# Kernel optimization log

Hardware: AMD Instinct MI355X
Metric: run time of the kernel (lower is better)

The kernel has to match this reference:

```python
import jax, jax.numpy as jnp
import numpy as np

N_TOKENS = 8192      # codebook size K
HIDDEN = 256         # hidden_size H
N = 8192             # batch of latent vectors (vmapped dim)
COMMITMENT_COST = 0.25


def setup_inputs() -> dict:
    key = jax.random.key(0)
    k_h, k_cb, _ = jax.random.split(key, 3)
    h = jax.random.normal(k_h, (N, HIDDEN), dtype=jnp.float32)
    # codebook initialized exactly as in __init__: normal * 0.1
    codebook = jax.random.normal(k_cb, (N_TOKENS, HIDDEN), dtype=jnp.float32) * 0.1
    temperature = jnp.ones((), dtype=jnp.float32)  # unused, API compat
    return {"h": h, "temperature": temperature, "codebook": codebook}


def reference(h, temperature, codebook):
    """Batched VQ quantization: one-hot nearest-codebook weights + commitment loss.

    h: (N, H) float32, codebook: (K, H) float32. Returns (hard (N,K), loss (N,)).
    """
    del temperature  # VQ is always hard; kept for API compatibility
    K = codebook.shape[0]
    # squared distances ||h - c||^2 = ||h||^2 - 2 h.c + ||c||^2, avoids (N,K,H) tensor
    h_sq = jnp.sum(h * h, axis=-1, keepdims=True)              # (N, 1)
    c_sq = jnp.sum(codebook * codebook, axis=-1)               # (K,)
    dists = h_sq - 2.0 * jnp.einsum('nh,kh->nk', h, codebook) + c_sq[None, :]  # (N, K)
    idx = jnp.argmin(dists, axis=-1)                           # (N,)
    hard = jax.nn.one_hot(idx, K, dtype=h.dtype)               # (N, K)
    # STE wrapping from __call__ (gradient of hard is zero anyway)
    hard = jax.lax.stop_gradient(hard)
    # commitment_loss (per token), matching the module's method
    z_q = codebook[idx]                                        # (N, H) gather
    codebook_loss = jnp.mean((jax.lax.stop_gradient(h) - z_q) ** 2, axis=-1)
    commit_loss = jnp.mean((h - jax.lax.stop_gradient(z_q)) ** 2, axis=-1)
    loss = codebook_loss + COMMITMENT_COST * commit_loss       # (N,)
    return hard, loss
```

## Files before the change

### kernel.cpp

```cpp
#include <hip/hip_runtime.h>
#include <hip/hip_bf16.h>
#include <math.h>

#define N_ROWS   8192
#define K_CODES  8192
#define H_DIM    256
#define NSPLIT2  32
#define MARGIN   5e-4f

typedef short short8 __attribute__((ext_vector_type(8)));
typedef float f32x4  __attribute__((ext_vector_type(4)));

#define C2_OFF      0
#define H2_OFF      8192
#define DISTF_OFF   16384
#define IDXF_OFF    (DISTF_OFF + 8192)
#define FCNT_OFF    (IDXF_OFF + 8192)
#define FLIST_OFF   (FCNT_OFF + 16)
#define MAXSLOT     64
#define WS_ZERO_BYTES ((size_t)(FLIST_OFF + MAXSLOT) * 4)

#define PK_AHI ((size_t)0)
#define PK_ALO ((size_t)4 << 20)
#define PK_BHI ((size_t)8 << 20)
#define PK_BLO ((size_t)12 << 20)
#define PART_BEST ((size_t)16 << 20)
#define PART_SEC  (PART_BEST + (size_t)(NSPLIT2 * N_ROWS * 4))
#define PART_IDX  (PART_SEC  + (size_t)(NSPLIT2 * N_ROWS * 4))
#define FIXP_BEST (PART_IDX  + (size_t)(NSPLIT2 * N_ROWS * 4))
#define FIXP_IDX  (FIXP_BEST + (size_t)(MAXSLOT * 64 * 8))
#define SCRATCH_BYTES ((size_t)0x1310000)

__device__ __forceinline__ void async_copy16(const void* g, void* l) {
    __builtin_amdgcn_global_load_lds(
        (const __attribute__((address_space(1))) unsigned int*)g,
        (__attribute__((address_space(3))) unsigned int*)l, 16, 0, 0);
}

__device__ __forceinline__ void conv2(float a, float b, unsigned& hi, unsigned& lo) {
    float2 p0 = make_float2(a, b);
    __hip_bfloat162 hb = __float22bfloat162_rn(p0);
    unsigned h = *(unsigned*)&hb;
    hi = h;
    float ra = a - __uint_as_float(h << 16);
    float rb = b - __uint_as_float(h & 0xFFFF0000u);
    float2 p1 = make_float2(ra, rb);
    __hip_bfloat162 lb = __float22bfloat162_rn(p1);
    lo = *(unsigned*)&lb;
}

__global__ __launch_bounds__(256) void pack_kernel(const float* __restrict__ h,
                                                   const float* __restrict__ cb,
                                                   char* __restrict__ out,
                                                   float* __restrict__ ws) {
    int w    = threadIdx.x >> 6;
    int lane = threadIdx.x & 63;
    int ln15 = lane & 15;
    int kg   = lane >> 4;
    bool isB = blockIdx.x >= 1024;
    int u = ((blockIdx.x & 1023) << 2) + w;
    int p = u >> 3, c = u & 7;
    const float* src = isB ? cb : h;
    char* hiB = out + (isB ? PK_BHI : PK_AHI);
    char* loB = out + (isB ? PK_BLO : PK_ALO);
    const float* s = src + (size_t)(p * 16 + ln15) * H_DIM + c * 32 + kg * 8;
    float4 v0 = *(const float4*)s;
    float4 v1 = *(const float4*)(s + 4);
    unsigned h0, h1, h2, h3, l0, l1, l2, l3;
    conv2(v0.x, v0.y, h0, l0);
    conv2(v0.z, v0.w, h1, l1);
    conv2(v1.x, v1.y, h2, l2);
    conv2(v1.z, v1.w, h3, l3);
    size_t off = ((size_t)u * 64 + lane) * 16;
    *(uint4*)(hiB + off) = make_uint4(h0, h1, h2, h3);
    *(uint4*)(loB + off) = make_uint4(l0, l1, l2, l3);

    float sq = v0.x*v0.x + v0.y*v0.y + v0.z*v0.z + v0.w*v0.w
             + v1.x*v1.x + v1.y*v1.y + v1.z*v1.z + v1.w*v1.w;
    sq += __shfl_xor(sq, 16, 64);
    sq += __shfl_xor(sq, 32, 64);
    if (kg == 0) {
        int row = p * 16 + ln15;
        atomicAdd(&ws[(isB ? C2_OFF : H2_OFF) + row], sq);
    }
}

__global__ __launch_bounds__(512, 2) void vq_min_kernel(const char* __restrict__ pk,
                                                        const float* __restrict__ c2g,
                                                        float* __restrict__ pbest,
                                                        float* __restrict__ psec,
                                                        int* __restrict__ pidx) {
    __shared__ __align__(16) char smem[131072];
    const int tid  = threadIdx.x;
    const int w    = tid >> 6;
    const int lane = tid & 63;
    const int ln15 = lane & 15;
    const int kg   = lane >> 4;
    const int wr   = w >> 2;
    const int wc   = w & 3;
    const int wr8  = wr * 8;
    const int wc4  = wc * 4;

    const int pA0 = blockIdx.x * 16;
    const int pB0 = blockIdx.y * 16;

    f32x4 acc[8][4];
    #pragma unroll
    for (int m = 0; m < 8; ++m)
        #pragma unroll
        for (int n = 0; n < 4; ++n) acc[m][n] = (f32x4){0.f, 0.f, 0.f, 0.f};

#define STAGE(sE, bufc) do {                                                   \
    const int ss_ = (sE);                                                      \
    const int tt_ = ss_ >> 3, cc_ = ss_ & 7;                                   \
    const char* Ab_ = pk + ((tt_ == 1) ? PK_ALO : PK_AHI);                     \
    const char* Bb_ = pk + ((tt_ == 2) ? PK_BLO : PK_BHI);                     \
    char* db_ = smem + (bufc) * 32768;                                         \
    async_copy16(Ab_ + (((size_t)(pA0 + 2*w)     * 8 + cc_) * 64 + lane) * 16, \
                 db_ + (2*w)     * 1024);                                      \
    async_copy16(Ab_ + (((size_t)(pA0 + 2*w + 1) * 8 + cc_) * 64 + lane) * 16, \
                 db_ + (2*w + 1) * 1024);                                      \
    async_copy16(Bb_ + (((size_t)(pB0 + 2*w)     * 8 + cc_) * 64 + lane) * 16, \
                 db_ + 16384 + (2*w)     * 1024);                              \
    async_copy16(Bb_ + (((size_t)(pB0 + 2*w + 1) * 8 + cc_) * 64 + lane) * 16, \
                 db_ + 16384 + (2*w + 1) * 1024);                              \
} while (0)

#define COMPUTE(bufc) do {                                                     \
    const char* sb_ = smem + (bufc) * 32768;                                   \
    short8 av[8], bv[4];                                                       \
    _Pragma("unroll")                                                          \
    for (int m = 0; m < 8; ++m)                                                \
        av[m] = *(const short8*)(sb_ + (wr8 + m) * 1024 + lane * 16);          \
    _Pragma("unroll")                                                          \
    for (int n = 0; n < 4; ++n)                                                \
        bv[n] = *(const short8*)(sb_ + 16384 + (wc4 + n) * 1024 + lane * 16);  \
    __builtin_amdgcn_s_setprio(1);                                             \
    _Pragma("unroll")                                                          \
    for (int m = 0; m < 8; ++m)                                                \
        _Pragma("unroll")                                                      \
        for (int n = 0; n < 4; ++n)                                            \
            acc[m][n] = __builtin_amdgcn_mfma_f32_16x16x32_bf16(               \
                av[m], bv[n], acc[m][n], 0, 0, 0);                             \
    __builtin_amdgcn_s_setprio(0);                                             \
} while (0)

#define ITER(sE, bufc, vm) do {                                                \
    if ((sE) + 2 < 24) STAGE((sE) + 2, ((bufc) + 2) & 3);                      \
    asm volatile("s_waitcnt vmcnt(" #vm ")" ::: "memory");                     \
    __builtin_amdgcn_sched_barrier(0);                                         \
    __builtin_amdgcn_s_barrier();                                              \
    __builtin_amdgcn_sched_barrier(0);                                         \
    COMPUTE(bufc);                                                             \
    __builtin_amdgcn_sched_barrier(0);                                         \
} while (0)

    STAGE(0, 0);
    STAGE(1, 1);

    #pragma unroll 1
    for (int sb = 0; sb < 20; sb += 4) {
        ITER(sb + 0, 0, 8);
        ITER(sb + 1, 1, 8);
        ITER(sb + 2, 2, 8);
        ITER(sb + 3, 3, 8);
    }
    ITER(20, 0, 8);
    ITER(21, 1, 8);
    ITER(22, 2, 4);
    ITER(23, 3, 0);

#undef ITER
#undef COMPUTE
#undef STAGE

    const int colbase = blockIdx.y * 256 + wc * 64;
    float cv[4];
    #pragma unroll
    for (int n = 0; n < 4; ++n) cv[n] = c2g[colbase + n * 16 + ln15];

    float* mbv = (float*)smem;
    float* msv = (float*)(smem + 4096);
    int*   miv = (int*)(smem + 8192);

    #pragma unroll
    for (int m = 0; m < 8; ++m) {
        #pragma unroll
        for (int reg = 0; reg < 4; ++reg) {
            float b = 3.4e38f, s2 = 3.4e38f;
            int   bi = 0;
            #pragma unroll
            for (int n = 0; n < 4; ++n) {
                float d = cv[n] - 2.f * acc[m][n][reg];
                int   k = colbase + n * 16 + ln15;
                if (d < b)       { s2 = b; b = d; bi = k; }
                else if (d < s2) { s2 = d; }
            }
            #pragma unroll
            for (int msk = 1; msk <= 8; msk <<= 1) {
                float ob = __shfl_xor(b, msk, 64);
                float os = __shfl_xor(s2, msk, 64);
                int   oi = __shfl_xor(bi, msk, 64);
                if (ob < b)      { s2 = fminf(b, os); b = ob; bi = oi; }
                else if (ob > b) { s2 = fminf(s2, ob); }
                else             { if (oi < bi) bi = oi; s2 = b; }
            }
            if (ln15 == 0) {
                int r = wr * 128 + m * 16 + kg * 4 + reg;
                mbv[r * 4 + wc] = b;
                msv[r * 4 + wc] = s2;
                miv[r * 4 + wc] = bi;
            }
        }
    }
    __syncthreads();
    if (tid < 256) {
        float b  = mbv[tid * 4];
        float s2 = msv[tid * 4];
        int   bi = miv[tid * 4];
        #pragma unroll
        for (int q = 1; q < 4; ++q) {
            float ob = mbv[tid * 4 + q];
            float os = msv[tid * 4 + q];
            int   oi = miv[tid * 4 + q];
            if (ob < b)      { s2 = fminf(b, os); b = ob; bi = oi; }
            else if (ob > b) { s2 = fminf(s2, ob); }
            else             { if (oi < bi) bi = oi; s2 = b; }
        }
        int grow = blockIdx.x * 256 + tid;
        pbest[(size_t)blockIdx.y * N_ROWS + grow] = b;
        psec [(size_t)blockIdx.y * N_ROWS + grow] = s2;
        pidx [(size_t)blockIdx.y * N_ROWS + grow] = bi;
    }
}

__global__ __launch_bounds__(256) void merge_kernel(const float* __restrict__ pbest,
                                                    const float* __restrict__ psec,
                                                    const int* __restrict__ pidx,
                                                    float* __restrict__ ws) {
    int row = blockIdx.x * blockDim.x + threadIdx.x;
    if (row >= N_ROWS) return;
    float b  = pbest[row];
    float s2 = psec[row];
    int   bi = pidx[row];
    for (int s = 1; s < NSPLIT2; s++) {
        float ob = pbest[s * N_ROWS + row];
        float os = psec [s * N_ROWS + row];
        int   oi = pidx [s * N_ROWS + row];
        if (ob < b)      { s2 = fminf(b, os); b = ob; bi = oi; }
        else if (ob > b) { s2 = fminf(s2, ob); }
        else             { if (oi < bi) bi = oi; s2 = b; }
    }
    float h2 = ws[H2_OFF + row];
    ws[DISTF_OFF + row] = h2 + b;
    ((int*)ws)[IDXF_OFF + row] = bi;
    if (s2 - b <= MARGIN) {
        int slot = atomicAdd(&((int*)ws)[FCNT_OFF], 1);
        if (slot < MAXSLOT) ((int*)ws)[FLIST_OFF + slot] = row;
    }
}

__global__ __launch_bounds__(256) void fixup_part(const float* __restrict__ h,
                                                  const float* __restrict__ cb,
                                                  float* __restrict__ ws,
                                                  double* __restrict__ fbest,
                                                  int* __restrict__ fidx) {
    int slot = blockIdx.y;
    int n = ((const int*)ws)[FCNT_OFF];
    if (n > MAXSLOT) n = MAXSLOT;
    if (slot >= n) return;
    int row   = ((const int*)ws)[FLIST_OFF + slot];
    int base  = blockIdx.x * 128;
    int wv    = threadIdx.x >> 6;
    int lane  = threadIdx.x & 63;
    float4 hv = *(const float4*)(h + (size_t)row * H_DIM + lane * 4);

    double best = 1e300;
    int    bi   = 1 << 30;
    for (int c = base + wv; c < base + 128; c += 4) {
        float4 cv = *(const float4*)(cb + (size_t)c * H_DIM + lane * 4);
        float dx = hv.x - cv.x, dy = hv.y - cv.y, dz = hv.z - cv.z, dw = hv.w - cv.w;
        double s = (double)dx * dx + (double)dy * dy + (double)dz * dz + (double)dw * dw;
        #pragma unroll
        for (int off = 32; off > 0; off >>= 1) s += __shfl_down(s, off, 64);
        if (lane == 0 && s < best) { best = s; bi = c; }
    }
    __shared__ double sb[4];
    __shared__ int    si[4];
    if (lane == 0) { sb[wv] = best; si[wv] = bi; }
    __syncthreads();
    if (threadIdx.x == 0) {
        double b = sb[0]; int x = si[0];
        for (int t = 1; t < 4; t++)
            if (sb[t] < b || (sb[t] == b && si[t] < x)) { b = sb[t]; x = si[t]; }
        fbest[slot * 64 + blockIdx.x] = b;
        fidx [slot * 64 + blockIdx.x] = x;
    }
}

__global__ __launch_bounds__(64) void fixup_final(float* __restrict__ ws,
                                                  const double* __restrict__ fbest,
                                                  const int* __restrict__ fidx) {
    int slot = blockIdx.x;
    int n = ((const int*)ws)[FCNT_OFF];
    if (n > MAXSLOT) n = MAXSLOT;
    if (slot >= n) return;
    int lane = threadIdx.x;
    double b = fbest[slot * 64 + lane];
    int    x = fidx [slot * 64 + lane];
    #pragma unroll
    for (int off = 32; off > 0; off >>= 1) {
        double ob = __shfl_down(b, off, 64);
        int    oi = __shfl_down(x, off, 64);
        if (ob < b || (ob == b && oi < x)) { b = ob; x = oi; }
    }
    if (lane == 0) {
        int row = ((const int*)ws)[FLIST_OFF + slot];
        ws[DISTF_OFF + row] = (float)b;
        ((int*)ws)[IDXF_OFF + row] = x;
    }
}

__global__ __launch_bounds__(256) void scatter_kernel(const float* __restrict__ ws,
                                                      float* __restrict__ out) {
    int row = blockIdx.x * 256 + threadIdx.x;
    int bi  = ((const int*)ws)[IDXF_OFF + row];
    out[(size_t)row * K_CODES + bi] = 1.0f;
    out[(size_t)N_ROWS * K_CODES + row] = (1.25f / 256.f) * ws[DISTF_OFF + row];
}

extern "C" void kernel_launch(void* const* d_in, const int* in_sizes, int n_in,
                              void* d_out, int out_size, void* d_ws, size_t ws_size,
                              hipStream_t stream) {
    const float* h  = (const float*)d_in[0];
    const float* cb = (const float*)d_in[2];
    float* out = (float*)d_out;
    float* ws  = (float*)d_ws;
    char*  pk  = (char*)d_out;

    float*  pbest = (float*)(pk + PART_BEST);
    float*  psec  = (float*)(pk + PART_SEC);
    int*    pidx  = (int*)(pk + PART_IDX);
    double* fbest = (double*)(pk + FIXP_BEST);
    int*    fidx  = (int*)(pk + FIXP_IDX);

    hipMemsetAsync(d_ws, 0, WS_ZERO_BYTES, stream);
    pack_kernel<<<2048, 256, 0, stream>>>(h, cb, pk, ws);
    vq_min_kernel<<<dim3(N_ROWS / 256, NSPLIT2), 512, 0, stream>>>(pk, ws, pbest, psec, pidx);
    merge_kernel<<<N_ROWS / 256, 256, 0, stream>>>(pbest, psec, pidx, ws);
    fixup_part<<<dim3(64, MAXSLOT), 256, 0, stream>>>(h, cb, ws, fbest, fidx);
    fixup_final<<<MAXSLOT, 64, 0, stream>>>(ws, fbest, fidx);
    hipMemsetAsync(d_out, 0, SCRATCH_BYTES, stream);
    scatter_kernel<<<N_ROWS / 256, 256, 0, stream>>>(ws, out);
}
```

Baseline: 440.5 us.

## Deepen LDS prefetch to three stages and split MFMA step into interleaved halves

```diff
diff --git a/kernel.cpp b/kernel.cpp
--- a/kernel.cpp
+++ b/kernel.cpp
@@ -35,6 +35,13 @@
     __builtin_amdgcn_global_load_lds(
         (const __attribute__((address_space(1))) unsigned int*)g,
         (__attribute__((address_space(3))) unsigned int*)l, 16, 0, 0);
+}
+
+template<int N> __device__ __forceinline__ void vmgate() {
+    if constexpr (N == 8)      asm volatile("s_waitcnt vmcnt(8)" ::: "memory");
+    else if constexpr (N == 4) asm volatile("s_waitcnt vmcnt(4)" ::: "memory");
+    else if constexpr (N == 0) asm volatile("s_waitcnt vmcnt(0)" ::: "memory");
+    if constexpr (N >= 0) __builtin_amdgcn_sched_barrier(0);
 }
 
 __device__ __forceinline__ void conv2(float a, float b, unsigned& hi, unsigned& lo) {
@@ -110,69 +117,98 @@
         #pragma unroll
         for (int n = 0; n < 4; ++n) acc[m][n] = (f32x4){0.f, 0.f, 0.f, 0.f};
 
-#define STAGE(sE, bufc) do {                                                   \
-    const int ss_ = (sE);                                                      \
-    const int tt_ = ss_ >> 3, cc_ = ss_ & 7;                                   \
-    const char* Ab_ = pk + ((tt_ == 1) ? PK_ALO : PK_AHI);                     \
-    const char* Bb_ = pk + ((tt_ == 2) ? PK_BLO : PK_BHI);                     \
-    char* db_ = smem + (bufc) * 32768;                                         \
-    async_copy16(Ab_ + (((size_t)(pA0 + 2*w)     * 8 + cc_) * 64 + lane) * 16, \
-                 db_ + (2*w)     * 1024);                                      \
-    async_copy16(Ab_ + (((size_t)(pA0 + 2*w + 1) * 8 + cc_) * 64 + lane) * 16, \
-                 db_ + (2*w + 1) * 1024);                                      \
-    async_copy16(Bb_ + (((size_t)(pB0 + 2*w)     * 8 + cc_) * 64 + lane) * 16, \
-                 db_ + 16384 + (2*w)     * 1024);                              \
-    async_copy16(Bb_ + (((size_t)(pB0 + 2*w + 1) * 8 + cc_) * 64 + lane) * 16, \
-                 db_ + 16384 + (2*w + 1) * 1024);                              \
+    short8 av_[4], bv_[4];
+
+#define STAGE_A(sE, dstb) do {                                                 \
+    const int ssA_ = (sE);                                                     \
+    const int ccA_ = ssA_ & 7;                                                 \
+    const char* Ab_ = pk + (((ssA_ >> 3) == 1) ? PK_ALO : PK_AHI);             \
+    char* dbA_ = smem + (dstb) * 32768;                                        \
+    async_copy16(Ab_ + (((size_t)(pA0 + 2*w)     * 8 + ccA_) * 64 + lane) * 16,\
+                 dbA_ + (2*w)     * 1024);                                     \
+    async_copy16(Ab_ + (((size_t)(pA0 + 2*w + 1) * 8 + ccA_) * 64 + lane) * 16,\
+                 dbA_ + (2*w + 1) * 1024);                                     \
 } while (0)
 
-#define COMPUTE(bufc) do {                                                     \
-    const char* sb_ = smem + (bufc) * 32768;                                   \
-    short8 av[8], bv[4];                                                       \
-    _Pragma("unroll")                                                          \
-    for (int m = 0; m < 8; ++m)                                                \
-        av[m] = *(const short8*)(sb_ + (wr8 + m) * 1024 + lane * 16);          \
-    _Pragma("unroll")                                                          \
-    for (int n = 0; n < 4; ++n)                                                \
-        bv[n] = *(const short8*)(sb_ + 16384 + (wc4 + n) * 1024 + lane * 16);  \
+#define STAGE_B(sE, dstb) do {                                                 \
+    const int ssB_ = (sE);                                                     \
+    const int ccB_ = ssB_ & 7;                                                 \
+    const char* Bb_ = pk + (((ssB_ >> 3) == 2) ? PK_BLO : PK_BHI);             \
+    char* dbB_ = smem + (dstb) * 32768 + 16384;                                \
+    async_copy16(Bb_ + (((size_t)(pB0 + 2*w)     * 8 + ccB_) * 64 + lane) * 16,\
+                 dbB_ + (2*w)     * 1024);                                     \
+    async_copy16(Bb_ + (((size_t)(pB0 + 2*w + 1) * 8 + ccB_) * 64 + lane) * 16,\
+                 dbB_ + (2*w + 1) * 1024);                                     \
+} while (0)
+
+#define STEP(sE, bufc, vmN, doStage) do {                                      \
+       \
+    {                                                                          \
+        const char* sa_ = smem + (bufc) * 32768;                               \
+        _Pragma("unroll")                                                      \
+        for (int m = 0; m < 4; ++m)                                            \
+            av_[m] = *(const short8*)(sa_ + (wr8 + m) * 1024 + lane * 16);     \
+        _Pragma("unroll")                                                      \
+        for (int n = 0; n < 4; ++n)                                            \
+            bv_[n] = *(const short8*)(sa_ + 16384 + (wc4 + n) * 1024 + lane * 16); \
+    }                                                                          \
+    if (doStage) STAGE_A((sE) + 3, ((bufc) + 3) & 3);                          \
+    __builtin_amdgcn_s_barrier();                                              \
+    asm volatile("s_waitcnt lgkmcnt(0)" ::: "memory");                         \
+    __builtin_amdgcn_sched_barrier(0);                                         \
     __builtin_amdgcn_s_setprio(1);                                             \
     _Pragma("unroll")                                                          \
-    for (int m = 0; m < 8; ++m)                                                \
+    for (int m = 0; m < 4; ++m)                                                \
         _Pragma("unroll")                                                      \
         for (int n = 0; n < 4; ++n)                                            \
             acc[m][n] = __builtin_amdgcn_mfma_f32_16x16x32_bf16(               \
-                av[m], bv[n], acc[m][n], 0, 0, 0);                             \
+                av_[m], bv_[n], acc[m][n], 0, 0, 0);                           \
     __builtin_amdgcn_s_setprio(0);                                             \
+    __builtin_amdgcn_s_barrier();                                              \
+     \
+    {                                                                          \
+        const char* sa_ = smem + (bufc) * 32768;                               \
+        _Pragma("unroll")                                                      \
+        for (int m = 0; m < 4; ++m)                                            \
+            av_[m] = *(const short8*)(sa_ + (wr8 + 4 + m) * 1024 + lane * 16); \
+    }                                                                          \
+    if (doStage) STAGE_B((sE) + 3, ((bufc) + 3) & 3);                          \
+    vmgate<vmN>();                                                             \
+    __builtin_amdgcn_s_barrier();                                              \
+    asm volatile("s_waitcnt lgkmcnt(0)" ::: "memory");                         \
+    __builtin_amdgcn_sched_barrier(0);                                         \
+    __builtin_amdgcn_s_setprio(1);                                             \
+    _Pragma("unroll")                                                          \
+    for (int m = 0; m < 4; ++m)                                                \
+        _Pragma("unroll")                                                      \
+        for (int n = 0; n < 4; ++n)                                            \
+            acc[4 + m][n] = __builtin_amdgcn_mfma_f32_16x16x32_bf16(           \
+                av_[m], bv_[n], acc[4 + m][n], 0, 0, 0);                       \
+    __builtin_amdgcn_s_setprio(0);                                             \
+    __builtin_amdgcn_s_barrier();                                              \
 } while (0)
 
-#define ITER(sE, bufc, vm) do {                                                \
-    if ((sE) + 2 < 24) STAGE((sE) + 2, ((bufc) + 2) & 3);                      \
-    asm volatile("s_waitcnt vmcnt(" #vm ")" ::: "memory");                     \
-    __builtin_amdgcn_sched_barrier(0);                                         \
-    __builtin_amdgcn_s_barrier();                                              \
-    __builtin_amdgcn_sched_barrier(0);                                         \
-    COMPUTE(bufc);                                                             \
-    __builtin_amdgcn_sched_barrier(0);                                         \
-} while (0)
-
-    STAGE(0, 0);
-    STAGE(1, 1);
+    STAGE_A(0, 0); STAGE_B(0, 0);
+    STAGE_A(1, 1); STAGE_B(1, 1);
+    STAGE_A(2, 2); STAGE_B(2, 2);
+    vmgate<8>();
+    __builtin_amdgcn_s_barrier();
 
     #pragma unroll 1
     for (int sb = 0; sb < 20; sb += 4) {
-        ITER(sb + 0, 0, 8);
-        ITER(sb + 1, 1, 8);
-        ITER(sb + 2, 2, 8);
-        ITER(sb + 3, 3, 8);
-    }
-    ITER(20, 0, 8);
-    ITER(21, 1, 8);
-    ITER(22, 2, 4);
-    ITER(23, 3, 0);
-
-#undef ITER
-#undef COMPUTE
-#undef STAGE
+        STEP(sb + 0, 0, 8, 1);
+        STEP(sb + 1, 1, 8, 1);
+        STEP(sb + 2, 2, 8, 1);
+        STEP(sb + 3, 3, 8, 1);
+    }
+    STEP(20, 0, 8, 1);
+    STEP(21, 1, 4, 0);
+    STEP(22, 2, 0, 0);
+    STEP(23, 3, -1, 0);
+
+#undef STEP
+#undef STAGE_B
+#undef STAGE_A
 
     const int colbase = blockIdx.y * 256 + wc * 64;
     float cv[4];
```

After: 448.2 us. Within noise of the previous version (+1.7%).
